# Performance work log

Measured on AMD Instinct MI355X. Metric: run time of the kernel, lower is better.

Reference implementation:

```python
import jax, jax.numpy as jnp
import numpy as np

N_EMBED = 4096
N_Q_HEADS = 32
N_KV_HEADS = 8
HEAD_DIM = N_EMBED // N_Q_HEADS  # 128
N_GROUPS = N_Q_HEADS // N_KV_HEADS  # 4
ROPE_BASE = 10000.0
BATCH, SEQ = 1, 2048


def setup_inputs() -> dict:
    key = jax.random.key(0)
    ks = jax.random.split(key, 5)
    hidden_state = jax.random.normal(ks[0], (BATCH, SEQ, N_EMBED), dtype=jnp.float32)
    # additive causal mask: 0 on/below diagonal, -inf above (SDPA float-mask semantics)
    causal = jnp.tril(jnp.ones((SEQ, SEQ), dtype=bool))
    attention_mask = jnp.where(causal, 0.0, -jnp.inf).astype(jnp.float32)[None, None]
    position_ids = jnp.arange(SEQ, dtype=jnp.int32)[None, :].repeat(BATCH, axis=0)
    s = 0.02
    Wq = jax.random.normal(ks[1], (N_EMBED, N_EMBED), dtype=jnp.float32) * s
    Wk = jax.random.normal(ks[2], (N_KV_HEADS * HEAD_DIM, N_EMBED), dtype=jnp.float32) * s
    Wv = jax.random.normal(ks[3], (N_KV_HEADS * HEAD_DIM, N_EMBED), dtype=jnp.float32) * s
    Wo = jax.random.normal(ks[4], (N_EMBED, N_EMBED), dtype=jnp.float32) * s
    return {"hidden_state": hidden_state, "attention_mask": attention_mask,
            "position_ids": position_ids, "Wq": Wq, "Wk": Wk, "Wv": Wv, "Wo": Wo}


def _rope_tables(position_ids):
    # mimic torch: inv_freq built in fp16 then used as float
    exponent = (jnp.arange(0, HEAD_DIM, 2, dtype=jnp.float16) / HEAD_DIM)
    inv_freq = (1.0 / (ROPE_BASE ** exponent)).astype(jnp.float32)  # [hd/2]
    m = position_ids.astype(jnp.float32)  # [bs, seq]
    m_theta = m[:, :, None] * inv_freq[None, None, :]  # [bs, seq, hd/2]
    m_theta = jnp.concatenate([m_theta, m_theta], axis=-1)  # [bs, seq, hd]
    return jnp.cos(m_theta), jnp.sin(m_theta)


def _rotate_half(x):
    half = x.shape[-1] // 2
    return jnp.concatenate([-x[..., half:], x[..., :half]], axis=-1)


def reference(hidden_state, attention_mask, position_ids, Wq, Wk, Wv, Wo):
    bs, seq, _ = hidden_state.shape
    q = (hidden_state @ Wq.T).reshape(bs, seq, N_Q_HEADS, HEAD_DIM).transpose(0, 2, 1, 3)
    k = (hidden_state @ Wk.T).reshape(bs, seq, N_KV_HEADS, HEAD_DIM).transpose(0, 2, 1, 3)
    v = (hidden_state @ Wv.T).reshape(bs, seq, N_KV_HEADS, HEAD_DIM).transpose(0, 2, 1, 3)

    cos, sin = _rope_tables(position_ids)
    cos, sin = cos[:, None], sin[:, None]  # broadcast over heads
    q = q * cos + _rotate_half(q) * sin
    k = k * cos + _rotate_half(k) * sin

    # GQA: group query heads per KV head instead of materializing KV copies
    qg = q.reshape(bs, N_KV_HEADS, N_GROUPS, seq, HEAD_DIM)
    scale = 1.0 / jnp.sqrt(jnp.float32(HEAD_DIM))
    scores = jnp.einsum('bhgqd,bhkd->bhgqk', qg, k) * scale + attention_mask[:, :, None]
    probs = jax.nn.softmax(scores, axis=-1)
    attn = jnp.einsum('bhgqk,bhkd->bhgqd', probs, v)  # [bs, kvh, g, seq, hd]
    attn = attn.reshape(bs, N_Q_HEADS, seq, HEAD_DIM).transpose(0, 2, 1, 3).reshape(bs, seq, N_EMBED)
    return attn @ Wo.T
```

## Files before the change

kernel.cpp:

```cpp
#include <hip/hip_runtime.h>
#include <hip/hip_bf16.h>

#define SEQ 2048
#define LDQKV 6144

typedef __attribute__((ext_vector_type(8))) __bf16 bf16x8;
typedef __attribute__((ext_vector_type(4))) __bf16 bf16x4;
typedef __attribute__((ext_vector_type(4))) float f32x4;

__device__ __forceinline__ void gload_lds16(const void* g, void* l) {
  __builtin_amdgcn_global_load_lds((__attribute__((address_space(1))) void*)(g),
                                   (__attribute__((address_space(3))) void*)(l), 16, 0, 0);
}

struct CvtArgs {
  const float* src0; const float* src1; const float* src2; const float* src3; const float* src4;
  __bf16* dst0; __bf16* dst1; __bf16* dst2; __bf16* dst3; __bf16* dst4;
};
__global__ __launch_bounds__(256) void cvt_all(CvtArgs a) {
  int b = blockIdx.x;
  const float* s; __bf16* d; int boff;
  if (b < 4096)       { s = a.src0; d = a.dst0; boff = b; }
  else if (b < 12288) { s = a.src1; d = a.dst1; boff = b - 4096; }
  else if (b < 14336) { s = a.src2; d = a.dst2; boff = b - 12288; }
  else if (b < 16384) { s = a.src3; d = a.dst3; boff = b - 14336; }
  else                { s = a.src4; d = a.dst4; boff = b - 16384; }
  long i = ((long)boff * 256 + threadIdx.x) * 8;
  f32x4 v0 = *(const f32x4*)(s + i);
  f32x4 v1 = *(const f32x4*)(s + i + 4);
  bf16x8 o;
  #pragma unroll
  for (int j = 0; j < 4; ++j) { o[j] = (__bf16)v0[j]; o[j + 4] = (__bf16)v1[j]; }
  *(bf16x8*)(d + i) = o;
}

__global__ __launch_bounds__(256) void rope_tab_k(const int* __restrict__ pos,
                                                  float* __restrict__ tab) {
  int i = blockIdx.x * 256 + threadIdx.x;
  int s = i >> 6, j = i & 63;
  float p = (float)pos[s];
  float pw = powf(10000.0f, (float)j * (1.0f / 64.0f));
  _Float16 ph = (_Float16)pw;
  _Float16 ivh = (_Float16)(1.0f / (float)ph);
  float freq = (float)ivh;
  float th = p * freq;
  tab[i] = cosf(th);
  tab[SEQ * 64 + i] = sinf(th);
}

__global__ __launch_bounds__(256) void rope_apply_k(__bf16* __restrict__ qkv,
                                                    const float* __restrict__ tab) {
  int i = blockIdx.x * 256 + threadIdx.x;
  int dc = i & 7;
  int ht = (i >> 3) % 40;
  int s = i / 320;
  long col = (ht < 32) ? (long)ht * 128 : (long)4096 + (long)(ht - 32) * 128;
  __bf16* p = qkv + (long)s * LDQKV + col + dc * 8;
  bf16x8 lo = *(bf16x8*)p;
  bf16x8 hi = *(bf16x8*)(p + 64);
  const float* tc = tab + (long)s * 64 + dc * 8;
  const float* ts = tc + SEQ * 64;
  bf16x8 lo2, hi2;
  #pragma unroll
  for (int e = 0; e < 8; ++e) {
    float c = tc[e], sn = ts[e];
    float lv = (float)lo[e], hv = (float)hi[e];
    lo2[e] = (__bf16)(lv * c - hv * sn);
    hi2[e] = (__bf16)(hv * c + lv * sn);
  }
  *(bf16x8*)p = lo2;
  *(bf16x8*)(p + 64) = hi2;
}

template<int BN, bool OUT_BF16>
__global__ __launch_bounds__(512, 2) void gemm8(const __bf16* __restrict__ A,
                                                const __bf16* __restrict__ B,
                                                void* __restrict__ C,
                                                int K, int ldc) {
  constexpr int BHR = BN / 2;
  constexpr int NFR = BN / 128;
  constexpr int LB  = BHR / 64;
  constexpr int NW  = 1 + LB;
  extern __shared__ __bf16 lds[];
  __bf16* Ab = lds;
  __bf16* Bb = lds + 16384;

  const int tid = threadIdx.x;
  const int wave = tid >> 6, lane = tid & 63;
  const int l15 = lane & 15, l4 = lane >> 4;
  const int wm = wave >> 2, wn = wave & 3;

  const int orig = blockIdx.x;
  const int swz = (orig & 7) * 32 + (orig >> 3);
  const int bx = swz & 15, by = swz >> 4;
  const long brow = (long)bx * 128, bcol = (long)by * BN;

  const int rS = tid >> 3;
  const int cS = ((tid & 7) * 8) ^ ((rS & 7) << 3);
  const int NT = K >> 6;

  auto stageA = [&](int buf, int qm, int t) {
    const __bf16* src = A + (brow + qm * 64 + rS) * (long)K + t * 64 + cS;
    gload_lds16(src, Ab + (buf * 2 + qm) * 4096 + wave * 512);
  };
  auto stageB = [&](int buf, int qn, int t) {
    #pragma unroll
    for (int i = 0; i < LB; ++i) {
      const __bf16* src = B + (bcol + qn * BHR + i * 64 + rS) * (long)K + t * 64 + cS;
      gload_lds16(src, Bb + (buf * 2 + qn) * (BHR * 64) + i * 4096 + wave * 512);
    }
  };

  bf16x8 afLo[2][2], afHi[2][2], b0[NFR][2], b1[NFR][2];
  auto readA = [&](bf16x8 (&dst)[2][2], int buf, int qm) {
    #pragma unroll
    for (int mi = 0; mi < 2; ++mi) {
      int r = wm * 32 + mi * 16 + l15;
      #pragma unroll
      for (int kf = 0; kf < 2; ++kf) {
        int c = (kf * 32 + l4 * 8) ^ ((r & 7) << 3);
        dst[mi][kf] = *(const bf16x8*)&Ab[(buf * 2 + qm) * 4096 + r * 64 + c];
      }
    }
  };
  auto readB = [&](bf16x8 (&dst)[NFR][2], int buf, int qn) {
    #pragma unroll
    for (int ni = 0; ni < NFR; ++ni) {
      int r = wn * (BN / 8) + ni * 16 + l15;
      #pragma unroll
      for (int kf = 0; kf < 2; ++kf) {
        int c = (kf * 32 + l4 * 8) ^ ((r & 7) << 3);
        dst[ni][kf] = *(const bf16x8*)&Bb[(buf * 2 + qn) * (BHR * 64) + r * 64 + c];
      }
    }
  };

  f32x4 acc[2][2][2][NFR] = {};
  auto mfmaQ = [&](bf16x8 (&af)[2][2], bf16x8 (&bf_)[NFR][2], f32x4 (&ac)[2][NFR]) {
    __builtin_amdgcn_s_setprio(1);
    #pragma unroll
    for (int mi = 0; mi < 2; ++mi)
      #pragma unroll
      for (int ni = 0; ni < NFR; ++ni)
        #pragma unroll
        for (int kf = 0; kf < 2; ++kf)
          ac[mi][ni] = __builtin_amdgcn_mfma_f32_16x16x32_bf16(af[mi][kf], bf_[ni][kf], ac[mi][ni], 0, 0, 0);
    __builtin_amdgcn_s_setprio(0);
  };

  #define VM_WAIT() do { \
    if constexpr (NW == 4) asm volatile("s_waitcnt vmcnt(4)" ::: "memory"); \
    else                   asm volatile("s_waitcnt vmcnt(3)" ::: "memory"); \
  } while (0)
  #define PH_BAR() do { __builtin_amdgcn_s_barrier(); __builtin_amdgcn_sched_barrier(0); } while (0)

  stageA(0, 0, 0); stageB(0, 0, 0); stageA(0, 1, 0); stageB(0, 1, 0);
  VM_WAIT();
  PH_BAR();

  for (int t = 0; t < NT; ++t) {
    const int buf = t & 1, nb = buf ^ 1;
    const bool pf = (t + 1 < NT);
    if (pf) stageA(nb, 0, t + 1);
    readA(afLo, buf, 0); readB(b0, buf, 0);
    mfmaQ(afLo, b0, acc[0][0]);
    VM_WAIT();
    PH_BAR();
    if (pf) stageB(nb, 0, t + 1);
    readA(afHi, buf, 1);
    mfmaQ(afHi, b0, acc[1][0]);
    VM_WAIT();
    PH_BAR();
    if (pf) stageA(nb, 1, t + 1);
    readB(b1, buf, 1);
    mfmaQ(afHi, b1, acc[1][1]);
    PH_BAR();
    if (pf) stageB(nb, 1, t + 1);
    mfmaQ(afLo, b1, acc[0][1]);
    VM_WAIT();
    PH_BAR();
  }
  #undef VM_WAIT
  #undef PH_BAR

  #pragma unroll
  for (int qm = 0; qm < 2; ++qm)
    #pragma unroll
    for (int qn = 0; qn < 2; ++qn)
      #pragma unroll
      for (int mi = 0; mi < 2; ++mi)
        #pragma unroll
        for (int ni = 0; ni < NFR; ++ni)
          #pragma unroll
          for (int j = 0; j < 4; ++j) {
            long rr = brow + qm * 64 + wm * 32 + mi * 16 + l4 * 4 + j;
            long cc = bcol + qn * BHR + wn * (BN / 8) + ni * 16 + l15;
            float v = acc[qm][qn][mi][ni][j];
            if (OUT_BF16) ((__bf16*)C)[rr * ldc + cc] = (__bf16)v;
            else          ((float*)C)[rr * ldc + cc] = v;
          }
}

__global__ __launch_bounds__(256) void flash_k(const __bf16* __restrict__ qkv,
                                               __bf16* __restrict__ ctx) {
  __shared__ __align__(16) __bf16 Kl[8192];
  __shared__ __align__(16) __bf16 Vt[8192];
  __shared__ __align__(16) __bf16 Pl[4][1024];

  const int bid = blockIdx.x;
  const int h = bid & 31;
  const int qt = 31 - (bid >> 5);
  const int kvh = h >> 2;
  const int q0 = qt * 64;
  const int tid = threadIdx.x, wave = tid >> 6, lane = tid & 63;
  const int l15 = lane & 15, l4 = lane >> 4;
  const int d2 = tid & 63, grp = tid >> 6;

  const __bf16* Qp = qkv + (long)h * 128;
  const __bf16* Kp = qkv + 4096 + (long)kvh * 128;
  const __bf16* Vp = qkv + 5120 + (long)kvh * 128;

  bf16x8 aq[4];
  {
    long qr = q0 + wave * 16 + l15;
    #pragma unroll
    for (int ks = 0; ks < 4; ++ks)
      aq[ks] = *(const bf16x8*)(Qp + qr * LDQKV + ks * 32 + l4 * 8);
  }
  f32x4 accO[8] = {};
  float lsum[4] = {0.f, 0.f, 0.f, 0.f};
  const float cexp = 0.08838834764831845f * 1.4426950408889634f;

  for (int kv0 = 0; kv0 <= q0; kv0 += 64) {
    __syncthreads();
    #pragma unroll
    for (int i = 0; i < 4; ++i) {
      int fo = i * 2048 + wave * 512 + lane * 8;
      int r = fo >> 7, c = fo & 127;
      int cs = c ^ ((r & 7) << 3);
      gload_lds16(Kp + (long)(kv0 + r) * LDQKV + cs, &Kl[i * 2048 + wave * 512]);
    }
    unsigned int vv[2][8];
    #pragma unroll
    for (int rep = 0; rep < 2; ++rep) {
      int cch = grp * 2 + rep;
      #pragma unroll
      for (int i = 0; i < 8; ++i)
        vv[rep][i] = *(const unsigned int*)(Vp + (long)(kv0 + cch * 8 + i) * LDQKV + 2 * d2);
    }
    #pragma unroll
    for (int rep = 0; rep < 2; ++rep) {
      int cch = grp * 2 + rep;
      #pragma unroll
      for (int half = 0; half < 2; ++half) {
        bf16x8 w;
        #pragma unroll
        for (int i = 0; i < 8; ++i)
          w[i] = __builtin_bit_cast(__bf16, (unsigned short)(vv[rep][i] >> (16 * half)));
        int d = 2 * d2 + half;
        *(bf16x8*)&Vt[d * 64 + ((cch * 8) ^ ((d2 & 7) * 8))] = w;
      }
    }
    __syncthreads();

    f32x4 s[4];
    #pragma unroll
    for (int t = 0; t < 4; ++t) s[t] = f32x4{0.f, 0.f, 0.f, 0.f};
    __builtin_amdgcn_s_setprio(1);
    #pragma unroll
    for (int t = 0; t < 4; ++t) {
      int r = t * 16 + l15;
      #pragma unroll
      for (int ks = 0; ks < 4; ++ks) {
        bf16x8 bk = *(const bf16x8*)&Kl[r * 128 + ((ks * 32 + l4 * 8) ^ ((r & 7) << 3))];
        s[t] = __builtin_amdgcn_mfma_f32_16x16x32_bf16(aq[ks], bk, s[t], 0, 0, 0);
      }
    }
    __builtin_amdgcn_s_setprio(0);

    const bool lastStep = (kv0 == q0);
    float pout[4][4];
    #pragma unroll
    for (int t = 0; t < 4; ++t)
      #pragma unroll
      for (int j = 0; j < 4; ++j) {
        float p = exp2f(s[t][j] * cexp);
        if (lastStep) {
          int qg = wave * 16 + l4 * 4 + j;
          int kg = t * 16 + l15;
          if (kg > qg) p = 0.f;
        }
        pout[t][j] = p;
      }
    #pragma unroll
    for (int j = 0; j < 4; ++j)
      lsum[j] += (pout[0][j] + pout[1][j]) + (pout[2][j] + pout[3][j]);

    #pragma unroll
    for (int t = 0; t < 4; ++t)
      #pragma unroll
      for (int j = 0; j < 4; ++j) {
        int r = l4 * 4 + j;
        int c = t * 16 + l15;
        Pl[wave][r * 64 + (c ^ ((r & 7) << 3))] = (__bf16)pout[t][j];
      }
    asm volatile("s_waitcnt lgkmcnt(0)" ::: "memory");
    __builtin_amdgcn_sched_barrier(0);
    bf16x8 ap[2];
    #pragma unroll
    for (int ks2 = 0; ks2 < 2; ++ks2) {
      int c = ks2 * 32 + l4 * 8;
      ap[ks2] = *(const bf16x8*)&Pl[wave][l15 * 64 + (c ^ ((l15 & 7) << 3))];
    }
    __builtin_amdgcn_s_setprio(1);
    #pragma unroll
    for (int dt = 0; dt < 8; ++dt) {
      int d = dt * 16 + l15;
      #pragma unroll
      for (int ks2 = 0; ks2 < 2; ++ks2) {
        int c = (ks2 * 32 + l4 * 8) ^ (((l15 >> 1) & 7) * 8);
        bf16x8 bv = *(const bf16x8*)&Vt[d * 64 + c];
        accO[dt] = __builtin_amdgcn_mfma_f32_16x16x32_bf16(ap[ks2], bv, accO[dt], 0, 0, 0);
      }
    }
    __builtin_amdgcn_s_setprio(0);
  }
  float rls[4];
  #pragma unroll
  for (int j = 0; j < 4; ++j) {
    float ls = lsum[j];
    ls += __shfl_xor(ls, 1, 16);
    ls += __shfl_xor(ls, 2, 16);
    ls += __shfl_xor(ls, 4, 16);
    ls += __shfl_xor(ls, 8, 16);
    rls[j] = 1.f / ls;
  }
  #pragma unroll
  for (int dt = 0; dt < 8; ++dt)
    #pragma unroll
    for (int j = 0; j < 4; ++j) {
      long qr = q0 + wave * 16 + l4 * 4 + j;
      long cc = (long)h * 128 + dt * 16 + l15;
      ctx[qr * 4096 + cc] = (__bf16)(accO[dt][j] * rls[j]);
    }
}

extern "C" void kernel_launch(void* const* d_in, const int* in_sizes, int n_in,
                              void* d_out, int out_size, void* d_ws, size_t ws_size,
                              hipStream_t stream) {
  const float* hs  = (const float*)d_in[0];
  const int*   pos = (const int*)d_in[2];
  const float* Wq  = (const float*)d_in[3];
  const float* Wk  = (const float*)d_in[4];
  const float* Wv  = (const float*)d_in[5];
  const float* Wo  = (const float*)d_in[6];
  char* ws = (char*)d_ws;
  __bf16* hsb  = (__bf16*)(ws + 0L);
  __bf16* wqkv = (__bf16*)(ws + 16777216L);
  __bf16* wob  = (__bf16*)(ws + 67108864L);
  __bf16* qkvb = (__bf16*)(ws + 100663296L);
  float*  tab  = (float*)(ws + 125829120L);
  __bf16* ctx  = (__bf16*)(ws + 126877696L);

  (void)hipFuncSetAttribute(reinterpret_cast<const void*>(&gemm8<384, true>),
                            hipFuncAttributeMaxDynamicSharedMemorySize, 131072);
  (void)hipFuncSetAttribute(reinterpret_cast<const void*>(&gemm8<256, false>),
                            hipFuncAttributeMaxDynamicSharedMemorySize, 98304);

  CvtArgs ca;
  ca.src0 = hs;  ca.dst0 = hsb;
  ca.src1 = Wq;  ca.dst1 = wqkv;
  ca.src2 = Wk;  ca.dst2 = wqkv + 16777216L;
  ca.src3 = Wv;  ca.dst3 = wqkv + 20971520L;
  ca.src4 = Wo;  ca.dst4 = wob;
  cvt_all<<<24576, 256, 0, stream>>>(ca);
  rope_tab_k<<<512, 256, 0, stream>>>(pos, tab);

  gemm8<384, true><<<256, 512, 131072, stream>>>(hsb, wqkv, qkvb, 4096, 6144);

  rope_apply_k<<<2560, 256, 0, stream>>>(qkvb, tab);

  flash_k<<<1024, 256, 0, stream>>>(qkvb, ctx);

  gemm8<256, false><<<256, 512, 98304, stream>>>(ctx, wob, d_out, 4096, 4096);
}
```

Before: 295.1 us.

## Use triple-buffered LDS pipeline for output projection GEMM

Replaces the double-buffered output projection GEMM with a dedicated kernel that keeps three LDS stages and prefetches two k-tiles ahead. Global-to-LDS loads for the next-next tile are interleaved between MFMA quadrants, and the waitcnt allows six loads to stay in flight. The aim is to hide global memory latency better in the final projection, at the cost of 144KB of LDS per block, which limits how many blocks can be resident per CU.

```diff
diff --git a/kernel.cpp b/kernel.cpp
--- a/kernel.cpp
+++ b/kernel.cpp
@@ -201,6 +201,120 @@
           }
 }
 
+__global__ __launch_bounds__(512, 2) void gemm3b(const __bf16* __restrict__ A,
+                                                 const __bf16* __restrict__ B,
+                                                 float* __restrict__ C,
+                                                 int K, int ldc) {
+  constexpr int BN = 256, BHR = 128, NFR = 2;
+  extern __shared__ __bf16 lds[];
+  const int tid = threadIdx.x;
+  const int wave = tid >> 6, lane = tid & 63;
+  const int l15 = lane & 15, l4 = lane >> 4;
+  const int wm = wave >> 2, wn = wave & 3;
+
+  const int orig = blockIdx.x;
+  const int swz = (orig & 7) * 32 + (orig >> 3);
+  const int bx = swz & 15, by = swz >> 4;
+  const long brow = (long)bx * 128, bcol = (long)by * BN;
+
+  const int rS = tid >> 3;
+  const int cS = ((tid & 7) * 8) ^ ((rS & 7) << 3);
+  const int NT = K >> 6;
+
+  auto bufbase = [&](int b3) -> __bf16* { return lds + b3 * 24576; };
+  auto stageA = [&](int b3, int qm, int t) {
+    gload_lds16(A + (brow + qm * 64 + rS) * (long)K + t * 64 + cS,
+                bufbase(b3) + qm * 4096 + wave * 512);
+  };
+  auto stageB = [&](int b3, int qn, int t) {
+    #pragma unroll
+    for (int i = 0; i < 2; ++i)
+      gload_lds16(B + (bcol + qn * BHR + i * 64 + rS) * (long)K + t * 64 + cS,
+                  bufbase(b3) + 8192 + qn * 8192 + i * 4096 + wave * 512);
+  };
+
+  bf16x8 afLo[2][2], afHi[2][2], b0[NFR][2], b1[NFR][2];
+  auto readA = [&](bf16x8 (&dst)[2][2], int b3, int qm) {
+    #pragma unroll
+    for (int mi = 0; mi < 2; ++mi) {
+      int r = wm * 32 + mi * 16 + l15;
+      #pragma unroll
+      for (int kf = 0; kf < 2; ++kf) {
+        int c = (kf * 32 + l4 * 8) ^ ((r & 7) << 3);
+        dst[mi][kf] = *(const bf16x8*)&bufbase(b3)[qm * 4096 + r * 64 + c];
+      }
+    }
+  };
+  auto readB = [&](bf16x8 (&dst)[NFR][2], int b3, int qn) {
+    #pragma unroll
+    for (int ni = 0; ni < NFR; ++ni) {
+      int r = wn * 32 + ni * 16 + l15;
+      #pragma unroll
+      for (int kf = 0; kf < 2; ++kf) {
+        int c = (kf * 32 + l4 * 8) ^ ((r & 7) << 3);
+        dst[ni][kf] = *(const bf16x8*)&bufbase(b3)[8192 + qn * 8192 + r * 64 + c];
+      }
+    }
+  };
+
+  f32x4 acc[2][2][2][NFR] = {};
+  auto mfmaQ = [&](bf16x8 (&af)[2][2], bf16x8 (&bf_)[NFR][2], f32x4 (&ac)[2][NFR]) {
+    __builtin_amdgcn_s_setprio(1);
+    #pragma unroll
+    for (int mi = 0; mi < 2; ++mi)
+      #pragma unroll
+      for (int ni = 0; ni < NFR; ++ni)
+        #pragma unroll
+        for (int kf = 0; kf < 2; ++kf)
+          ac[mi][ni] = __builtin_amdgcn_mfma_f32_16x16x32_bf16(af[mi][kf], bf_[ni][kf], ac[mi][ni], 0, 0, 0);
+    __builtin_amdgcn_s_setprio(0);
+  };
+
+  stageA(0, 0, 0); stageB(0, 0, 0); stageA(0, 1, 0); stageB(0, 1, 0);
+  stageA(1, 0, 1); stageB(1, 0, 1); stageA(1, 1, 1); stageB(1, 1, 1);
+  asm volatile("s_waitcnt vmcnt(6)" ::: "memory");
+  __builtin_amdgcn_s_barrier();
+  __builtin_amdgcn_sched_barrier(0);
+
+  for (int t = 0; t < NT; ++t) {
+    const int cur = t % 3, pre = (t + 2) % 3;
+    const bool pf2 = (t + 2 < NT);
+    if (pf2) stageA(pre, 0, t + 2);
+    readA(afLo, cur, 0); readB(b0, cur, 0);
+    mfmaQ(afLo, b0, acc[0][0]);
+    if (pf2) stageB(pre, 0, t + 2);
+    readA(afHi, cur, 1);
+    mfmaQ(afHi, b0, acc[1][0]);
+    if (pf2) stageA(pre, 1, t + 2);
+    readB(b1, cur, 1);
+    mfmaQ(afHi, b1, acc[1][1]);
+    if (pf2) stageB(pre, 1, t + 2);
+    mfmaQ(afLo, b1, acc[0][1]);
+    if (t + 1 < NT) {
+      __builtin_amdgcn_sched_barrier(0);
+      if (pf2) asm volatile("s_waitcnt vmcnt(6)" ::: "memory");
+      else     asm volatile("s_waitcnt vmcnt(0)" ::: "memory");
+      __builtin_amdgcn_s_barrier();
+      __builtin_amdgcn_sched_barrier(0);
+    }
+  }
+
+  #pragma unroll
+  for (int qm = 0; qm < 2; ++qm)
+    #pragma unroll
+    for (int qn = 0; qn < 2; ++qn)
+      #pragma unroll
+      for (int mi = 0; mi < 2; ++mi)
+        #pragma unroll
+        for (int ni = 0; ni < NFR; ++ni)
+          #pragma unroll
+          for (int j = 0; j < 4; ++j) {
+            long rr = brow + qm * 64 + wm * 32 + mi * 16 + l4 * 4 + j;
+            long cc = bcol + qn * BHR + wn * 32 + ni * 16 + l15;
+            C[rr * ldc + cc] = acc[qm][qn][mi][ni][j];
+          }
+}
+
 __global__ __launch_bounds__(256) void flash_k(const __bf16* __restrict__ qkv,
                                                __bf16* __restrict__ ctx) {
   __shared__ __align__(16) __bf16 Kl[8192];
@@ -364,8 +478,8 @@
 
   (void)hipFuncSetAttribute(reinterpret_cast<const void*>(&gemm8<384, true>),
                             hipFuncAttributeMaxDynamicSharedMemorySize, 131072);
-  (void)hipFuncSetAttribute(reinterpret_cast<const void*>(&gemm8<256, false>),
-                            hipFuncAttributeMaxDynamicSharedMemorySize, 98304);
+  (void)hipFuncSetAttribute(reinterpret_cast<const void*>(&gemm3b),
+                            hipFuncAttributeMaxDynamicSharedMemorySize, 147456);
 
   CvtArgs ca;
   ca.src0 = hs;  ca.dst0 = hsb;
@@ -382,5 +496,5 @@
 
   flash_k<<<1024, 256, 0, stream>>>(qkvb, ctx);
 
-  gemm8<256, false><<<256, 512, 98304, stream>>>(ctx, wob, d_out, 4096, 4096);
-}
+  gemm3b<<<256, 512, 147456, stream>>>(ctx, wob, (float*)d_out, 4096, 4096);
+}
```

After: 291.7 us. No clear change (-1.1%).

## Restructure GEMM pipeline to single barrier per K-tile with optional triple buffering

Applied to the files above, without the earlier changes.

Replaces the four-phase per-tile barrier schedule of the bf16 GEMM with a single barrier per K-tile, issuing the next tile's loads right after reading the current one. Adds a 3-buffer mode, used for the output projection, that prefetches two tiles ahead to hide global latency. Triple buffering raises LDS to 144KB per block, which likely reduces blocks per CU. The 2-buffer path now waits for all loads each tile, which can expose load latency.

```diff
diff --git a/kernel.cpp b/kernel.cpp
--- a/kernel.cpp
+++ b/kernel.cpp
@@ -72,18 +72,17 @@
   *(bf16x8*)(p + 64) = hi2;
 }
 
-template<int BN, bool OUT_BF16>
-__global__ __launch_bounds__(512, 2) void gemm8(const __bf16* __restrict__ A,
+template<int BN, int BUFS, bool OUT_BF16>
+__global__ __launch_bounds__(512, 2) void gemmW(const __bf16* __restrict__ A,
                                                 const __bf16* __restrict__ B,
                                                 void* __restrict__ C,
                                                 int K, int ldc) {
   constexpr int BHR = BN / 2;
   constexpr int NFR = BN / 128;
   constexpr int LB  = BHR / 64;
-  constexpr int NW  = 1 + LB;
+  constexpr int NA  = (BUFS == 3) ? 2 : 1;
+  constexpr int TE  = (128 + BN) * 64;
   extern __shared__ __bf16 lds[];
-  __bf16* Ab = lds;
-  __bf16* Bb = lds + 16384;
 
   const int tid = threadIdx.x;
   const int wave = tid >> 6, lane = tid & 63;
@@ -99,38 +98,38 @@
   const int cS = ((tid & 7) * 8) ^ ((rS & 7) << 3);
   const int NT = K >> 6;
 
-  auto stageA = [&](int buf, int qm, int t) {
-    const __bf16* src = A + (brow + qm * 64 + rS) * (long)K + t * 64 + cS;
-    gload_lds16(src, Ab + (buf * 2 + qm) * 4096 + wave * 512);
-  };
-  auto stageB = [&](int buf, int qn, int t) {
-    #pragma unroll
-    for (int i = 0; i < LB; ++i) {
-      const __bf16* src = B + (bcol + qn * BHR + i * 64 + rS) * (long)K + t * 64 + cS;
-      gload_lds16(src, Bb + (buf * 2 + qn) * (BHR * 64) + i * 4096 + wave * 512);
-    }
+  auto bufp = [&](int b) -> __bf16* { return lds + b * TE; };
+  auto stageA = [&](int b, int qm, int t) {
+    gload_lds16(A + (brow + qm * 64 + rS) * (long)K + t * 64 + cS,
+                bufp(b) + qm * 4096 + wave * 512);
+  };
+  auto stageB = [&](int b, int qn, int t) {
+    #pragma unroll
+    for (int i = 0; i < LB; ++i)
+      gload_lds16(B + (bcol + qn * BHR + i * 64 + rS) * (long)K + t * 64 + cS,
+                  bufp(b) + 8192 + qn * (BHR * 64) + i * 4096 + wave * 512);
   };
 
   bf16x8 afLo[2][2], afHi[2][2], b0[NFR][2], b1[NFR][2];
-  auto readA = [&](bf16x8 (&dst)[2][2], int buf, int qm) {
+  auto readA = [&](bf16x8 (&dst)[2][2], int b, int qm) {
     #pragma unroll
     for (int mi = 0; mi < 2; ++mi) {
       int r = wm * 32 + mi * 16 + l15;
       #pragma unroll
       for (int kf = 0; kf < 2; ++kf) {
         int c = (kf * 32 + l4 * 8) ^ ((r & 7) << 3);
-        dst[mi][kf] = *(const bf16x8*)&Ab[(buf * 2 + qm) * 4096 + r * 64 + c];
-      }
-    }
-  };
-  auto readB = [&](bf16x8 (&dst)[NFR][2], int buf, int qn) {
+        dst[mi][kf] = *(const bf16x8*)&bufp(b)[qm * 4096 + r * 64 + c];
+      }
+    }
+  };
+  auto readB = [&](bf16x8 (&dst)[NFR][2], int b, int qn) {
     #pragma unroll
     for (int ni = 0; ni < NFR; ++ni) {
       int r = wn * (BN / 8) + ni * 16 + l15;
       #pragma unroll
       for (int kf = 0; kf < 2; ++kf) {
         int c = (kf * 32 + l4 * 8) ^ ((r & 7) << 3);
-        dst[ni][kf] = *(const bf16x8*)&Bb[(buf * 2 + qn) * (BHR * 64) + r * 64 + c];
+        dst[ni][kf] = *(const bf16x8*)&bufp(b)[8192 + qn * (BHR * 64) + r * 64 + c];
       }
     }
   };
@@ -148,40 +147,39 @@
     __builtin_amdgcn_s_setprio(0);
   };
 
-  #define VM_WAIT() do { \
-    if constexpr (NW == 4) asm volatile("s_waitcnt vmcnt(4)" ::: "memory"); \
-    else                   asm volatile("s_waitcnt vmcnt(3)" ::: "memory"); \
-  } while (0)
-  #define PH_BAR() do { __builtin_amdgcn_s_barrier(); __builtin_amdgcn_sched_barrier(0); } while (0)
-
-  stageA(0, 0, 0); stageB(0, 0, 0); stageA(0, 1, 0); stageB(0, 1, 0);
-  VM_WAIT();
-  PH_BAR();
+  #pragma unroll
+  for (int tt = 0; tt < NA; ++tt) {
+    stageA(tt % BUFS, 0, tt); stageB(tt % BUFS, 0, tt);
+    stageA(tt % BUFS, 1, tt); stageB(tt % BUFS, 1, tt);
+  }
+  if constexpr (BUFS == 3) asm volatile("s_waitcnt vmcnt(6)" ::: "memory");
+  else                     asm volatile("s_waitcnt vmcnt(0)" ::: "memory");
+  __builtin_amdgcn_s_barrier();
+  __builtin_amdgcn_sched_barrier(0);
 
   for (int t = 0; t < NT; ++t) {
-    const int buf = t & 1, nb = buf ^ 1;
-    const bool pf = (t + 1 < NT);
-    if (pf) stageA(nb, 0, t + 1);
-    readA(afLo, buf, 0); readB(b0, buf, 0);
+    const int cur = t % BUFS, pre = (t + NA) % BUFS;
+    const bool pf = (t + NA < NT);
+    readA(afLo, cur, 0); readB(b0, cur, 0);
+    if (pf) { stageA(pre, 0, t + NA); stageB(pre, 0, t + NA); }
     mfmaQ(afLo, b0, acc[0][0]);
-    VM_WAIT();
-    PH_BAR();
-    if (pf) stageB(nb, 0, t + 1);
-    readA(afHi, buf, 1);
+    readA(afHi, cur, 1); readB(b1, cur, 1);
+    if (pf) { stageA(pre, 1, t + NA); stageB(pre, 1, t + NA); }
     mfmaQ(afHi, b0, acc[1][0]);
-    VM_WAIT();
-    PH_BAR();
-    if (pf) stageA(nb, 1, t + 1);
-    readB(b1, buf, 1);
     mfmaQ(afHi, b1, acc[1][1]);
-    PH_BAR();
-    if (pf) stageB(nb, 1, t + 1);
     mfmaQ(afLo, b1, acc[0][1]);
-    VM_WAIT();
-    PH_BAR();
-  }
-  #undef VM_WAIT
-  #undef PH_BAR
+    if (t + 1 < NT) {
+      __builtin_amdgcn_sched_barrier(0);
+      if constexpr (BUFS == 3) {
+        if (pf) asm volatile("s_waitcnt vmcnt(6)" ::: "memory");
+        else    asm volatile("s_waitcnt vmcnt(0)" ::: "memory");
+      } else {
+        asm volatile("s_waitcnt vmcnt(0)" ::: "memory");
+      }
+      __builtin_amdgcn_s_barrier();
+      __builtin_amdgcn_sched_barrier(0);
+    }
+  }
 
   #pragma unroll
   for (int qm = 0; qm < 2; ++qm)
@@ -362,10 +360,10 @@
   float*  tab  = (float*)(ws + 125829120L);
   __bf16* ctx  = (__bf16*)(ws + 126877696L);
 
-  (void)hipFuncSetAttribute(reinterpret_cast<const void*>(&gemm8<384, true>),
+  (void)hipFuncSetAttribute(reinterpret_cast<const void*>(&gemmW<384, 2, true>),
                             hipFuncAttributeMaxDynamicSharedMemorySize, 131072);
-  (void)hipFuncSetAttribute(reinterpret_cast<const void*>(&gemm8<256, false>),
-                            hipFuncAttributeMaxDynamicSharedMemorySize, 98304);
+  (void)hipFuncSetAttribute(reinterpret_cast<const void*>(&gemmW<256, 3, false>),
+                            hipFuncAttributeMaxDynamicSharedMemorySize, 147456);
 
   CvtArgs ca;
   ca.src0 = hs;  ca.dst0 = hsb;
@@ -376,11 +374,11 @@
   cvt_all<<<24576, 256, 0, stream>>>(ca);
   rope_tab_k<<<512, 256, 0, stream>>>(pos, tab);
 
-  gemm8<384, true><<<256, 512, 131072, stream>>>(hsb, wqkv, qkvb, 4096, 6144);
+  gemmW<384, 2, true><<<256, 512, 131072, stream>>>(hsb, wqkv, qkvb, 4096, 6144);
 
   rope_apply_k<<<2560, 256, 0, stream>>>(qkvb, tab);
 
   flash_k<<<1024, 256, 0, stream>>>(qkvb, ctx);
 
-  gemm8<256, false><<<256, 512, 98304, stream>>>(ctx, wob, d_out, 4096, 4096);
-}
+  gemmW<256, 3, false><<<256, 512, 147456, stream>>>(ctx, wob, d_out, 4096, 4096);
+}
```

After: 283.1 us (median of 3 runs). 4.1% less time.
